# Optimization experiments

Measured on AMD Instinct MI355X. Metric: run time of the kernel, lower is better.

The kernel has to match this reference:

```python
import jax, jax.numpy as jnp
import numpy as np

B, H, W, C_IN, C_OUT = 32, 128, 128, 128, 128
N_MODES = (32, 32)          # modes kept along each spatial axis
DEG, RANK = 2, 64
M_FRONT = (N_MODES[0] + 1) // 2   # 16: low positive-frequency modes on axis 0
M_BACK = N_MODES[0] - M_FRONT     # 16: high (negative-frequency) modes on axis 0
W_MODES = N_MODES[1] // 2 + 1     # 17: rfft half-spectrum modes on last axis


def _as_complex(p):
    # p: (..., 2) float -> complex
    return jax.lax.complex(p[..., 0], p[..., 1])


def setup_inputs() -> dict:
    key = jax.random.key(0)
    kx, k1, k2, k3, k4 = jax.random.split(key, 5)
    X = jax.random.normal(kx, (B, H, W, C_IN), dtype=jnp.float32)
    # torch.rand on cfloat -> uniform[0,1) real and imag parts
    kout0 = jax.random.uniform(k1, (N_MODES[0], 1, C_OUT, DEG, RANK, 2), dtype=jnp.float32)
    kin0  = jax.random.uniform(k2, (N_MODES[0], 1, C_IN,  DEG, RANK, 2), dtype=jnp.float32)
    kout1 = jax.random.uniform(k3, (1, W_MODES, C_OUT, DEG, RANK, 2), dtype=jnp.float32)
    kin1  = jax.random.uniform(k4, (1, W_MODES, C_IN,  DEG, RANK, 2), dtype=jnp.float32)
    return {"X": X, "kout0": kout0, "kin0": kin0, "kout1": kout1, "kin1": kin1}


def reference(X, kout0, kin0, kout1, kin1):
    ko0, ki0 = _as_complex(kout0), _as_complex(kin0)
    ko1, ki1 = _as_complex(kout1), _as_complex(kin1)
    # low-rank summand per spatial axis: (...idr, ...jdr -> ...ijd)
    S0 = jnp.einsum('...idr,...jdr->...ijd', ko0, ki0)   # (32, 1, O, I, D)
    S1 = jnp.einsum('...idr,...jdr->...ijd', ko1, ki1)   # (1, 17, O, I, D)
    # product over axes, sum over degree d: (32, 17, O, I)
    K = jnp.einsum('...ijd,...ijd->...ij', S0, S1)

    Xf = jnp.fft.rfftn(X, axes=(-3, -2), norm='forward')  # (B, H, W//2+1, C_in) complex
    Y = jnp.zeros(Xf.shape[:-1] + (K.shape[-2],), dtype=jnp.complex64)
    # quadrant 1: low modes on axis 0
    Y = Y.at[:, :M_FRONT, :W_MODES].set(
        jnp.einsum('hwij,bhwj->bhwi', K[:M_FRONT, :W_MODES], Xf[:, :M_FRONT, :W_MODES]))
    # quadrant 2: high (negative-frequency) modes on axis 0
    Y = Y.at[:, -M_BACK:, :W_MODES].set(
        jnp.einsum('hwij,bhwj->bhwi', K[-M_BACK:, :W_MODES], Xf[:, -M_BACK:, :W_MODES]))
    return jnp.fft.irfftn(Y, s=(H, W), axes=(-3, -2), norm='forward')
```

## Files before the change

kernel.cpp:

```cpp
#include <hip/hip_runtime.h>
#include <math.h>

#define PI2 6.283185307179586f


__global__ __launch_bounds__(128) void k_S(
    const float2* __restrict__ ko0, const float2* __restrict__ ki0,
    const float2* __restrict__ ko1, const float2* __restrict__ ki1,
    float2* __restrict__ S0, float2* __restrict__ S1) {
  int bid = blockIdx.x;
  int s = bid >> 7;
  int i = bid & 127;
  int j = threadIdx.x;
  const float2* ko; const float2* ki; float2* S; int si;
  if (s < 32) { ko = ko0; ki = ki0; S = S0; si = s; }
  else        { ko = ko1; ki = ki1; S = S1; si = s - 32; }
  __shared__ float2 koS[2][64];
  koS[j >> 6][j & 63] = ko[(si * 128 + i) * 128 + j];
  __syncthreads();
  const float2* kirow = ki + (si * 128 + j) * 128;
  float2 acc[2];
#pragma unroll
  for (int d = 0; d < 2; d++) {
    float2 a2 = make_float2(0.f, 0.f);
    for (int r = 0; r < 64; r++) {
      float2 a = koS[d][r];
      float2 b = kirow[d * 64 + r];
      a2.x += a.x * b.x - a.y * b.y;
      a2.y += a.x * b.y + a.y * b.x;
    }
    acc[d] = a2;
  }
  ((float4*)S)[(si * 128 + i) * 128 + j] =
      make_float4(acc[0].x, acc[0].y, acc[1].x, acc[1].y);
}

__global__ __launch_bounds__(256) void k_K(
    const float2* __restrict__ S0, const float2* __restrict__ S1,
    float2* __restrict__ K) {
  int tid = blockIdx.x * 256 + threadIdx.x;
  if (tid >= 544 * 16384) return;
  int m = tid >> 14;
  int ij = tid & 16383;
  int hm = m / 17, w = m - hm * 17;
  float4 a = ((const float4*)S0)[hm * 16384 + ij];
  float4 b = ((const float4*)S1)[w * 16384 + ij];
  float2 acc;
  acc.x = a.x * b.x - a.y * b.y + a.z * b.z - a.w * b.w;
  acc.y = a.x * b.y + a.y * b.x + a.z * b.w + a.w * b.z;
  K[tid] = acc;
}

__global__ __launch_bounds__(256) void k_F1(
    const float* __restrict__ X, float2* __restrict__ Xw) {
  __shared__ float2 tw[128];
  int t = threadIdx.x;
  if (t < 128) { float s, c; __sincosf(PI2 * t / 128.f, &s, &c); tw[t] = make_float2(c, s); }
  __syncthreads();
  int c = t & 127;
  int b = blockIdx.x >> 6;
  int y = (blockIdx.x & 63) * 2 + (t >> 7);
  const float* xrow = X + ((size_t)(b * 128 + y) * 128) * 128 + c;
  float2 acc[17];
#pragma unroll
  for (int k = 0; k < 17; k++) acc[k] = make_float2(0.f, 0.f);
  for (int x = 0; x < 128; x++) {
    float xv = xrow[x * 128];
#pragma unroll
    for (int k = 0; k < 17; k++) {
      float2 w = tw[(k * x) & 127];
      acc[k].x += xv * w.x;
      acc[k].y -= xv * w.y;
    }
  }
  const float sc = 1.f / 16384.f;
  float2* orow = Xw + ((size_t)(b * 128 + y) * 17) * 128 + c;
#pragma unroll
  for (int k = 0; k < 17; k++)
    orow[k * 128] = make_float2(acc[k].x * sc, acc[k].y * sc);
}

__global__ __launch_bounds__(256) void k_F2(
    const float2* __restrict__ Xw, float2* __restrict__ Xf) {
  __shared__ float2 tw[128];
  __shared__ float2 red[32 * 128];
  int t = threadIdx.x;
  if (t < 128) { float s, c; __sincosf(PI2 * t / 128.f, &s, &c); tw[t] = make_float2(c, s); }
  __syncthreads();
  int b = blockIdx.x / 17, k = blockIdx.x - b * 17;
  int c = t & 127, half = t >> 7;
  float2 acc[32];
#pragma unroll
  for (int hm = 0; hm < 32; hm++) acc[hm] = make_float2(0.f, 0.f);
  for (int yy = 0; yy < 64; yy++) {
    int y = half * 64 + yy;
    float2 xv = Xw[((size_t)(b * 128 + y) * 17 + k) * 128 + c];
#pragma unroll
    for (int hm = 0; hm < 32; hm++) {
      int h = hm < 16 ? hm : hm + 96;
      float2 w = tw[(h * y) & 127];
      acc[hm].x += xv.x * w.x + xv.y * w.y;
      acc[hm].y += xv.y * w.x - xv.x * w.y;
    }
  }
  if (half == 1) {
#pragma unroll
    for (int hm = 0; hm < 32; hm++) red[hm * 128 + c] = acc[hm];
  }
  __syncthreads();
  if (half == 0) {
#pragma unroll
    for (int hm = 0; hm < 32; hm++) {
      float2 o = red[hm * 128 + c];
      o.x += acc[hm].x; o.y += acc[hm].y;
      Xf[((size_t)(b * 32 + hm) * 17 + k) * 128 + c] = o;
    }
  }
}

__global__ __launch_bounds__(256) void k_spec(
    const float2* __restrict__ K, const float2* __restrict__ Xf,
    float2* __restrict__ Y) {
  __shared__ float2 Xs[32][128];
  __shared__ float2 Ks[16][129];
  int m = blockIdx.x;
  int hm = m / 17, w = m - hm * 17;
  int t = threadIdx.x;
  for (int q = t; q < 32 * 128; q += 256) {
    int b = q >> 7, j = q & 127;
    Xs[b][j] = Xf[((size_t)(b * 32 + hm) * 17 + w) * 128 + j];
  }
  int i = t & 127, bh = t >> 7;
  float2 acc[16];
#pragma unroll
  for (int bb = 0; bb < 16; bb++) acc[bb] = make_float2(0.f, 0.f);
  const float2* Km = K + (size_t)m * 16384;
  for (int jt = 0; jt < 128; jt += 16) {
    __syncthreads();
    for (int q = t; q < 16 * 128; q += 256) {
      int ii = q >> 4, jj = q & 15;
      Ks[jj][ii] = Km[ii * 128 + jt + jj];
    }
    __syncthreads();
#pragma unroll 4
    for (int jj = 0; jj < 16; jj++) {
      float2 kv = Ks[jj][i];
#pragma unroll
      for (int bb = 0; bb < 16; bb++) {
        float2 xv = Xs[bh * 16 + bb][jt + jj];
        acc[bb].x += kv.x * xv.x - kv.y * xv.y;
        acc[bb].y += kv.x * xv.y + kv.y * xv.x;
      }
    }
  }
#pragma unroll
  for (int bb = 0; bb < 16; bb++) {
    int b = bh * 16 + bb;
    Y[((size_t)(b * 32 + hm) * 17 + w) * 128 + i] = acc[bb];
  }
}

__global__ __launch_bounds__(256) void k_I1(
    const float2* __restrict__ Y, float2* __restrict__ Q) {
  __shared__ float2 tw[128];
  __shared__ float2 Ys[32][128];
  int t = threadIdx.x;
  if (t < 128) { float s, c; __sincosf(PI2 * t / 128.f, &s, &c); tw[t] = make_float2(c, s); }
  int b = blockIdx.x / 17, k = blockIdx.x - b * 17;
  for (int q = t; q < 32 * 128; q += 256) {
    int hm = q >> 7, o = q & 127;
    Ys[hm][o] = Y[((size_t)(b * 32 + hm) * 17 + k) * 128 + o];
  }
  __syncthreads();
  int o = t & 127, yh = t >> 7;
  for (int yy = 0; yy < 64; yy++) {
    int y = yh * 64 + yy;
    float2 acc = make_float2(0.f, 0.f);
#pragma unroll
    for (int hm = 0; hm < 32; hm++) {
      int h = hm < 16 ? hm : hm + 96;
      float2 w = tw[(h * y) & 127];
      float2 v = Ys[hm][o];
      acc.x += v.x * w.x - v.y * w.y;
      acc.y += v.x * w.y + v.y * w.x;
    }
    Q[((size_t)(b * 128 + y) * 17 + k) * 128 + o] = acc;
  }
}

__global__ __launch_bounds__(256) void k_I2(
    const float2* __restrict__ Q, float* __restrict__ out) {
  __shared__ float2 tw[128];
  __shared__ float2 Qs[17][128];
  int t = threadIdx.x;
  if (t < 128) { float s, c; __sincosf(PI2 * t / 128.f, &s, &c); tw[t] = make_float2(c, s); }
  int b = blockIdx.x >> 7, y = blockIdx.x & 127;
  for (int q = t; q < 17 * 128; q += 256) {
    int k = q >> 7, o = q & 127;
    float2 v = Q[((size_t)(b * 128 + y) * 17 + k) * 128 + o];
    float wgt = (k == 0) ? 1.f : 2.f;
    Qs[k][o] = make_float2(v.x * wgt, v.y * wgt);
  }
  __syncthreads();
  int o = t & 127, xh = t >> 7;
  float* orow = out + ((size_t)(b * 128 + y) * 128) * 128 + o;
  for (int xx = 0; xx < 64; xx++) {
    int x = xh * 64 + xx;
    float acc = 0.f;
#pragma unroll
    for (int k = 0; k < 17; k++) {
      float2 w = tw[(k * x) & 127];
      float2 v = Qs[k][o];
      acc += v.x * w.x - v.y * w.y;
    }
    orow[x * 128] = acc;
  }
}

extern "C" void kernel_launch(void* const* d_in, const int* in_sizes, int n_in,
                              void* d_out, int out_size, void* d_ws, size_t ws_size,
                              hipStream_t stream) {
  (void)in_sizes; (void)n_in; (void)out_size;
  const float*  X     = (const float*)d_in[0];
  const float2* kout0 = (const float2*)d_in[1];
  const float2* kin0  = (const float2*)d_in[2];
  const float2* kout1 = (const float2*)d_in[3];
  const float2* kin1  = (const float2*)d_in[4];
  float* out = (float*)d_out;

  const size_t NA = 8912896;
  const size_t need = (2 * NA + 4456448) * sizeof(float2);
  if (ws_size < need) return;
  float2* ws = (float2*)d_ws;
  float2* A  = ws;
  float2* K  = ws + NA;
  float2* C  = ws + 2 * NA;
  float2* S0 = C;
  float2* S1 = C + 1048576;
  float2* Xf = C;
  float2* Yk = C + 2228224;

  k_S   <<<49 * 128, 128, 0, stream>>>(kout0, kin0, kout1, kin1, S0, S1);
  k_F1  <<<32 * 64, 256, 0, stream>>>(X, A);
  k_K   <<<(544 * 16384) / 256, 256, 0, stream>>>(S0, S1, K);
  k_F2  <<<32 * 17, 256, 0, stream>>>(A, Xf);
  k_spec<<<544, 256, 0, stream>>>(K, Xf, Yk);
  k_I1  <<<32 * 17, 256, 0, stream>>>(Yk, A);
  k_I2  <<<32 * 128, 256, 0, stream>>>(A, out);
}
```

Measured before the change: 1.122 ms.

## Fuse K construction into spectral kernel and restructure DFT stage kernels

Removes the k_K kernel and its 70MB K buffer by computing K on the fly from S0 and S1 while loading tiles in k_spec. The DFT kernels are reworked: F1 and I2 each process two rows per thread to reuse twiddle loads, F2 splits modes across thread halves and drops the shared-memory reduction, and I1 keeps Y values in registers. Twiddle indexing now uses byte offsets. The trade-off is more register pressure and two S loads per K element in k_spec.

```diff
diff --git a/kernel.cpp b/kernel.cpp
--- a/kernel.cpp
+++ b/kernel.cpp
@@ -7,12 +7,12 @@
 __global__ __launch_bounds__(128) void k_S(
     const float2* __restrict__ ko0, const float2* __restrict__ ki0,
     const float2* __restrict__ ko1, const float2* __restrict__ ki1,
-    float2* __restrict__ S0, float2* __restrict__ S1) {
+    float4* __restrict__ S0, float4* __restrict__ S1) {
   int bid = blockIdx.x;
   int s = bid >> 7;
   int i = bid & 127;
   int j = threadIdx.x;
-  const float2* ko; const float2* ki; float2* S; int si;
+  const float2* ko; const float2* ki; float4* S; int si;
   if (s < 32) { ko = ko0; ki = ki0; S = S0; si = s; }
   else        { ko = ko1; ki = ki1; S = S1; si = s - 32; }
   __shared__ float2 koS[2][64];
@@ -31,24 +31,7 @@
     }
     acc[d] = a2;
   }
-  ((float4*)S)[(si * 128 + i) * 128 + j] =
-      make_float4(acc[0].x, acc[0].y, acc[1].x, acc[1].y);
-}
-
-__global__ __launch_bounds__(256) void k_K(
-    const float2* __restrict__ S0, const float2* __restrict__ S1,
-    float2* __restrict__ K) {
-  int tid = blockIdx.x * 256 + threadIdx.x;
-  if (tid >= 544 * 16384) return;
-  int m = tid >> 14;
-  int ij = tid & 16383;
-  int hm = m / 17, w = m - hm * 17;
-  float4 a = ((const float4*)S0)[hm * 16384 + ij];
-  float4 b = ((const float4*)S1)[w * 16384 + ij];
-  float2 acc;
-  acc.x = a.x * b.x - a.y * b.y + a.z * b.z - a.w * b.w;
-  acc.y = a.x * b.y + a.y * b.x + a.z * b.w + a.w * b.z;
-  K[tid] = acc;
+  S[(si * 128 + i) * 128 + j] = make_float4(acc[0].x, acc[0].y, acc[1].x, acc[1].y);
 }
 
 __global__ __launch_bounds__(256) void k_F1(
@@ -57,70 +40,71 @@
   int t = threadIdx.x;
   if (t < 128) { float s, c; __sincosf(PI2 * t / 128.f, &s, &c); tw[t] = make_float2(c, s); }
   __syncthreads();
-  int c = t & 127;
+  const char* twc = (const char*)tw;
+  int c = t & 127, kg = t >> 7;
   int b = blockIdx.x >> 6;
-  int y = (blockIdx.x & 63) * 2 + (t >> 7);
-  const float* xrow = X + ((size_t)(b * 128 + y) * 128) * 128 + c;
-  float2 acc[17];
-#pragma unroll
-  for (int k = 0; k < 17; k++) acc[k] = make_float2(0.f, 0.f);
+  int y0 = (blockIdx.x & 63) * 2;
+  const float* xr0 = X + ((size_t)(b * 128 + y0) * 128) * 128 + c;
+  const float* xr1 = xr0 + 16384;
+  float2 a0[9], a1[9];
+#pragma unroll
+  for (int kk = 0; kk < 9; kk++) { a0[kk] = make_float2(0.f, 0.f); a1[kk] = make_float2(0.f, 0.f); }
+  int kb8 = kg * 9 * 8;
   for (int x = 0; x < 128; x++) {
-    float xv = xrow[x * 128];
-#pragma unroll
-    for (int k = 0; k < 17; k++) {
-      float2 w = tw[(k * x) & 127];
-      acc[k].x += xv * w.x;
-      acc[k].y -= xv * w.y;
+    float v0 = xr0[x * 128];
+    float v1 = xr1[x * 128];
+#pragma unroll
+    for (int kk = 0; kk < 9; kk++) {
+      int ob = ((kb8 + kk * 8) * x) & 1016;
+      float2 w = *(const float2*)(twc + ob);
+      a0[kk].x += v0 * w.x; a0[kk].y -= v0 * w.y;
+      a1[kk].x += v1 * w.x; a1[kk].y -= v1 * w.y;
     }
   }
   const float sc = 1.f / 16384.f;
-  float2* orow = Xw + ((size_t)(b * 128 + y) * 17) * 128 + c;
-#pragma unroll
-  for (int k = 0; k < 17; k++)
-    orow[k * 128] = make_float2(acc[k].x * sc, acc[k].y * sc);
+  float2* o0 = Xw + ((size_t)(b * 128 + y0) * 17) * 128 + c;
+#pragma unroll
+  for (int kk = 0; kk < 9; kk++) {
+    int k = kg * 9 + kk;
+    if (k < 17) {
+      o0[k * 128] = make_float2(a0[kk].x * sc, a0[kk].y * sc);
+      o0[2176 + k * 128] = make_float2(a1[kk].x * sc, a1[kk].y * sc);
+    }
+  }
 }
 
 __global__ __launch_bounds__(256) void k_F2(
     const float2* __restrict__ Xw, float2* __restrict__ Xf) {
   __shared__ float2 tw[128];
-  __shared__ float2 red[32 * 128];
-  int t = threadIdx.x;
-  if (t < 128) { float s, c; __sincosf(PI2 * t / 128.f, &s, &c); tw[t] = make_float2(c, s); }
-  __syncthreads();
+  int t = threadIdx.x;
+  if (t < 128) { float s, c; __sincosf(PI2 * t / 128.f, &s, &c); tw[t] = make_float2(c, s); }
+  __syncthreads();
+  const char* twc = (const char*)tw;
   int b = blockIdx.x / 17, k = blockIdx.x - b * 17;
-  int c = t & 127, half = t >> 7;
-  float2 acc[32];
-#pragma unroll
-  for (int hm = 0; hm < 32; hm++) acc[hm] = make_float2(0.f, 0.f);
-  for (int yy = 0; yy < 64; yy++) {
-    int y = half * 64 + yy;
-    float2 xv = Xw[((size_t)(b * 128 + y) * 17 + k) * 128 + c];
-#pragma unroll
-    for (int hm = 0; hm < 32; hm++) {
-      int h = hm < 16 ? hm : hm + 96;
-      float2 w = tw[(h * y) & 127];
-      acc[hm].x += xv.x * w.x + xv.y * w.y;
-      acc[hm].y += xv.y * w.x - xv.x * w.y;
-    }
-  }
-  if (half == 1) {
-#pragma unroll
-    for (int hm = 0; hm < 32; hm++) red[hm * 128 + c] = acc[hm];
-  }
-  __syncthreads();
-  if (half == 0) {
-#pragma unroll
-    for (int hm = 0; hm < 32; hm++) {
-      float2 o = red[hm * 128 + c];
-      o.x += acc[hm].x; o.y += acc[hm].y;
-      Xf[((size_t)(b * 32 + hm) * 17 + k) * 128 + c] = o;
-    }
-  }
+  int c = t & 127, hh = t >> 7;
+  float2 acc[16];
+#pragma unroll
+  for (int q = 0; q < 16; q++) acc[q] = make_float2(0.f, 0.f);
+  int hb8 = hh ? 112 * 8 : 0;
+  const float2* xp = Xw + ((size_t)(b * 128) * 17 + k) * 128 + c;
+  for (int y = 0; y < 128; y++) {
+    float2 xv = xp[(size_t)y * 2176];
+#pragma unroll
+    for (int q = 0; q < 16; q++) {
+      int ob = ((hb8 + q * 8) * y) & 1016;
+      float2 w = *(const float2*)(twc + ob);
+      acc[q].x += xv.x * w.x + xv.y * w.y;
+      acc[q].y += xv.y * w.x - xv.x * w.y;
+    }
+  }
+  float2* op = Xf + ((size_t)(b * 32 + hh * 16) * 17 + k) * 128 + c;
+#pragma unroll
+  for (int q = 0; q < 16; q++) op[(size_t)q * 2176] = acc[q];
 }
 
 __global__ __launch_bounds__(256) void k_spec(
-    const float2* __restrict__ K, const float2* __restrict__ Xf,
-    float2* __restrict__ Y) {
+    const float4* __restrict__ S0, const float4* __restrict__ S1,
+    const float2* __restrict__ Xf, float2* __restrict__ Y) {
   __shared__ float2 Xs[32][128];
   __shared__ float2 Ks[16][129];
   int m = blockIdx.x;
@@ -130,16 +114,20 @@
     int b = q >> 7, j = q & 127;
     Xs[b][j] = Xf[((size_t)(b * 32 + hm) * 17 + w) * 128 + j];
   }
+  const float4* s0p = S0 + (size_t)hm * 16384;
+  const float4* s1p = S1 + (size_t)w * 16384;
   int i = t & 127, bh = t >> 7;
   float2 acc[16];
 #pragma unroll
   for (int bb = 0; bb < 16; bb++) acc[bb] = make_float2(0.f, 0.f);
-  const float2* Km = K + (size_t)m * 16384;
   for (int jt = 0; jt < 128; jt += 16) {
     __syncthreads();
     for (int q = t; q < 16 * 128; q += 256) {
       int ii = q >> 4, jj = q & 15;
-      Ks[jj][ii] = Km[ii * 128 + jt + jj];
+      float4 a = s0p[ii * 128 + jt + jj];
+      float4 b4 = s1p[ii * 128 + jt + jj];
+      Ks[jj][ii] = make_float2(a.x * b4.x - a.y * b4.y + a.z * b4.z - a.w * b4.w,
+                               a.x * b4.y + a.y * b4.x + a.z * b4.w + a.w * b4.z);
     }
     __syncthreads();
 #pragma unroll 4
@@ -163,57 +151,66 @@
 __global__ __launch_bounds__(256) void k_I1(
     const float2* __restrict__ Y, float2* __restrict__ Q) {
   __shared__ float2 tw[128];
-  __shared__ float2 Ys[32][128];
-  int t = threadIdx.x;
-  if (t < 128) { float s, c; __sincosf(PI2 * t / 128.f, &s, &c); tw[t] = make_float2(c, s); }
+  int t = threadIdx.x;
+  if (t < 128) { float s, c; __sincosf(PI2 * t / 128.f, &s, &c); tw[t] = make_float2(c, s); }
+  __syncthreads();
+  const char* twc = (const char*)tw;
   int b = blockIdx.x / 17, k = blockIdx.x - b * 17;
-  for (int q = t; q < 32 * 128; q += 256) {
-    int hm = q >> 7, o = q & 127;
-    Ys[hm][o] = Y[((size_t)(b * 32 + hm) * 17 + k) * 128 + o];
-  }
-  __syncthreads();
   int o = t & 127, yh = t >> 7;
+  float2 v[32];
+#pragma unroll
+  for (int hm = 0; hm < 32; hm++)
+    v[hm] = Y[((size_t)(b * 32 + hm) * 17 + k) * 128 + o];
+  float2* qp = Q + ((size_t)(b * 128) * 17 + k) * 128 + o;
   for (int yy = 0; yy < 64; yy++) {
     int y = yh * 64 + yy;
-    float2 acc = make_float2(0.f, 0.f);
+    float2 a = make_float2(0.f, 0.f);
 #pragma unroll
     for (int hm = 0; hm < 32; hm++) {
-      int h = hm < 16 ? hm : hm + 96;
-      float2 w = tw[(h * y) & 127];
-      float2 v = Ys[hm][o];
-      acc.x += v.x * w.x - v.y * w.y;
-      acc.y += v.x * w.y + v.y * w.x;
-    }
-    Q[((size_t)(b * 128 + y) * 17 + k) * 128 + o] = acc;
+      const int h8 = (hm < 16 ? hm : hm + 96) * 8;
+      int ob = (h8 * y) & 1016;
+      float2 w = *(const float2*)(twc + ob);
+      a.x += v[hm].x * w.x - v[hm].y * w.y;
+      a.y += v[hm].x * w.y + v[hm].y * w.x;
+    }
+    qp[(size_t)y * 2176] = a;
   }
 }
 
 __global__ __launch_bounds__(256) void k_I2(
     const float2* __restrict__ Q, float* __restrict__ out) {
   __shared__ float2 tw[128];
-  __shared__ float2 Qs[17][128];
-  int t = threadIdx.x;
-  if (t < 128) { float s, c; __sincosf(PI2 * t / 128.f, &s, &c); tw[t] = make_float2(c, s); }
-  int b = blockIdx.x >> 7, y = blockIdx.x & 127;
-  for (int q = t; q < 17 * 128; q += 256) {
-    int k = q >> 7, o = q & 127;
-    float2 v = Q[((size_t)(b * 128 + y) * 17 + k) * 128 + o];
+  int t = threadIdx.x;
+  if (t < 128) { float s, c; __sincosf(PI2 * t / 128.f, &s, &c); tw[t] = make_float2(c, s); }
+  __syncthreads();
+  const char* twc = (const char*)tw;
+  int b = blockIdx.x >> 6;
+  int y0 = (blockIdx.x & 63) * 2;
+  int o = t & 127, xh = t >> 7;
+  const float2* q0p = Q + ((size_t)(b * 128 + y0) * 17) * 128 + o;
+  float2 q0[17], q1[17];
+#pragma unroll
+  for (int k = 0; k < 17; k++) {
     float wgt = (k == 0) ? 1.f : 2.f;
-    Qs[k][o] = make_float2(v.x * wgt, v.y * wgt);
-  }
-  __syncthreads();
-  int o = t & 127, xh = t >> 7;
-  float* orow = out + ((size_t)(b * 128 + y) * 128) * 128 + o;
+    float2 v0 = q0p[k * 128];
+    float2 v1 = q0p[2176 + k * 128];
+    q0[k] = make_float2(v0.x * wgt, v0.y * wgt);
+    q1[k] = make_float2(v1.x * wgt, v1.y * wgt);
+  }
+  float* o0 = out + ((size_t)(b * 128 + y0) * 128) * 128 + o;
+  float* o1 = o0 + 16384;
   for (int xx = 0; xx < 64; xx++) {
     int x = xh * 64 + xx;
-    float acc = 0.f;
+    float s0 = 0.f, s1 = 0.f;
 #pragma unroll
     for (int k = 0; k < 17; k++) {
-      float2 w = tw[(k * x) & 127];
-      float2 v = Qs[k][o];
-      acc += v.x * w.x - v.y * w.y;
-    }
-    orow[x * 128] = acc;
+      int ob = (k * 8 * x) & 1016;
+      float2 w = *(const float2*)(twc + ob);
+      s0 += q0[k].x * w.x - q0[k].y * w.y;
+      s1 += q1[k].x * w.x - q1[k].y * w.y;
+    }
+    o0[x * 128] = s0;
+    o1[x * 128] = s1;
   }
 }
 
@@ -228,23 +225,21 @@
   const float2* kin1  = (const float2*)d_in[4];
   float* out = (float*)d_out;
 
+  float2* ws = (float2*)d_ws;
   const size_t NA = 8912896;
-  const size_t need = (2 * NA + 4456448) * sizeof(float2);
+  float2* A  = ws;
+  float2* S0 = ws + NA;
+  float2* S1 = S0 + 1048576;
+  float2* Xf = S1 + 557056;
+  float2* Yk = Xf + 2228224;
+  const size_t need = (NA + 1048576 + 557056 + 2 * 2228224) * sizeof(float2);
   if (ws_size < need) return;
-  float2* ws = (float2*)d_ws;
-  float2* A  = ws;
-  float2* K  = ws + NA;
-  float2* C  = ws + 2 * NA;
-  float2* S0 = C;
-  float2* S1 = C + 1048576;
-  float2* Xf = C;
-  float2* Yk = C + 2228224;
-
-  k_S   <<<49 * 128, 128, 0, stream>>>(kout0, kin0, kout1, kin1, S0, S1);
+
+  k_S   <<<49 * 128, 128, 0, stream>>>(kout0, kin0, kout1, kin1,
+                                       (float4*)S0, (float4*)S1);
   k_F1  <<<32 * 64, 256, 0, stream>>>(X, A);
-  k_K   <<<(544 * 16384) / 256, 256, 0, stream>>>(S0, S1, K);
   k_F2  <<<32 * 17, 256, 0, stream>>>(A, Xf);
-  k_spec<<<544, 256, 0, stream>>>(K, Xf, Yk);
+  k_spec<<<544, 256, 0, stream>>>((const float4*)S0, (const float4*)S1, Xf, Yk);
   k_I1  <<<32 * 17, 256, 0, stream>>>(Yk, A);
-  k_I2  <<<32 * 128, 256, 0, stream>>>(A, out);
-}
+  k_I2  <<<32 * 64, 256, 0, stream>>>(A, out);
+}
```

After: 1.045 ms. -6.9%, faster.
